# Kernel tuning notes

Measured on AMD Instinct MI355X. Metric: run time of the kernel, lower is better.

The kernel has to match this reference:

```python
import jax, jax.numpy as jnp
import numpy as np

N_NODES = 100000
N_GRAPHS = 256
EPS = 1e-5


def setup_inputs() -> dict:
    key = jax.random.key(0)
    ks = jax.random.split(key, 16)
    x = jax.random.normal(ks[0], (N_NODES, 7), dtype=jnp.float32)
    edge_index = jax.random.randint(ks[1], (2, 1600000), 0, N_NODES, dtype=jnp.int64)
    batch = jnp.sort(jax.random.randint(ks[2], (N_NODES,), 0, N_GRAPHS, dtype=jnp.int64))

    def lin(k, fi, fo):
        s = 1.0 / np.sqrt(fi)
        kw, kb = jax.random.split(k)
        W = jax.random.uniform(kw, (fi, fo), jnp.float32, -s, s)
        b = jax.random.uniform(kb, (fo,), jnp.float32, -s, s)
        return W, b

    W1, b1 = lin(ks[3], 7, 71)
    W2, b2 = lin(ks[4], 71, 135)
    W3, b3 = lin(ks[5], 135, 199)
    Wl1, bl1 = lin(ks[6], 199, 49)
    Wl2, bl2 = lin(ks[7], 49, 2)
    return {
        "x": x, "edge_index": edge_index, "batch": batch,
        "bn0_g": jnp.ones((7,)), "bn0_b": jnp.zeros((7,)),
        "bn1_g": jnp.ones((71,)), "bn1_b": jnp.zeros((71,)),
        "bn2_g": jnp.ones((135,)), "bn2_b": jnp.zeros((135,)),
        "W1": W1, "b1": b1, "W2": W2, "b2": b2, "W3": W3, "b3": b3,
        "Wl1": Wl1, "bl1": bl1, "Wl2": Wl2, "bl2": bl2,
    }


def _bn(x, g, b):
    # BatchNorm1d in training mode: batch stats over node dim
    m = jnp.mean(x, axis=0)
    v = jnp.mean(jnp.square(x - m), axis=0)
    return (x - m) * jax.lax.rsqrt(v + EPS) * g + b


def _gcn(x, src, dst, norm, W, b):
    # PyG GCNConv: x' = D^{-1/2} (A+I) D^{-1/2} (x W) + b
    h = x @ W
    out = jax.ops.segment_sum(norm[:, None] * h[src], dst, num_segments=N_NODES)
    return out + b


def reference(x, edge_index, batch, bn0_g, bn0_b, bn1_g, bn1_b, bn2_g, bn2_b,
              W1, b1, W2, b2, W3, b3, Wl1, bl1, Wl2, bl2):
    # add self loops
    loops = jnp.arange(N_NODES, dtype=edge_index.dtype)
    src = jnp.concatenate([edge_index[0], loops])
    dst = jnp.concatenate([edge_index[1], loops])
    deg = jax.ops.segment_sum(jnp.ones_like(dst, dtype=x.dtype), dst, num_segments=N_NODES)
    d_isqrt = jax.lax.rsqrt(jnp.maximum(deg, 1.0))
    norm = d_isqrt[src] * d_isqrt[dst]

    h = _bn(x, bn0_g, bn0_b)
    h = jax.nn.relu(_gcn(h, src, dst, norm, W1, b1))
    h = _bn(h, bn1_g, bn1_b)
    h = jax.nn.relu(_gcn(h, src, dst, norm, W2, b2))
    h = _bn(h, bn2_g, bn2_b)
    h = jax.nn.relu(_gcn(h, src, dst, norm, W3, b3))

    # global mean pool over graphs
    sums = jax.ops.segment_sum(h, batch, num_segments=N_GRAPHS)
    cnts = jax.ops.segment_sum(jnp.ones((h.shape[0],), h.dtype), batch, num_segments=N_GRAPHS)
    pooled = sums / jnp.maximum(cnts, 1.0)[:, None]

    out = pooled @ Wl1 + bl1
    out = out @ Wl2 + bl2
    return out
```

## Files before the change

### kernel.cpp

```cpp
#include <hip/hip_runtime.h>
#include <hip/hip_fp16.h>

#define EPSV 1e-5f
#define BIN_CH 4096
#define BCAP 8192

typedef _Float16 f16;
typedef f16 half8 __attribute__((ext_vector_type(8)));
typedef float f32x4 __attribute__((ext_vector_type(4)));


__global__ __launch_bounds__(256) void k_bin(const int* __restrict__ src,
                                             const int* __restrict__ dst, int E, int EN,
                                             int NBK, int* __restrict__ gcur,
                                             int* __restrict__ binned) {
    __shared__ int cnt[512];
    __shared__ int base[512];
    for (int b = threadIdx.x; b < 512; b += 256) cnt[b] = 0;
    __syncthreads();
    int i0 = blockIdx.x * BIN_CH;
    int i1 = i0 + BIN_CH; if (i1 > EN) i1 = EN;
    for (int i = i0 + threadIdx.x; i < i1; i += 256) {
        int d = (i < E) ? dst[i] : (i - E);
        atomicAdd(&cnt[d >> 8], 1);
    }
    __syncthreads();
    for (int b = threadIdx.x; b < NBK; b += 256)
        if (cnt[b]) base[b] = b * BCAP + atomicAdd(&gcur[b], cnt[b]);
    __syncthreads();
    for (int i = i0 + threadIdx.x; i < i1; i += 256) {
        int s, d;
        if (i < E) { s = src[i]; d = dst[i]; }
        else       { s = i - E; d = s; }
        int pos = atomicAdd(&base[d >> 8], 1);
        binned[pos] = s | ((d & 255) << 24);
    }
}

__global__ __launch_bounds__(256) void k_bucket(const int* __restrict__ binned,
                                                const int* __restrict__ gcur, int N,
                                                int* __restrict__ deg, int* __restrict__ rs,
                                                int* __restrict__ csr_s,
                                                float* __restrict__ disq) {
    __shared__ int deg_l[256];
    __shared__ int sc[256];
    __shared__ int cur_l[256];
    int b = blockIdx.x;
    int t = threadIdx.x;
    int start = b * BCAP, end = start + gcur[b];
    deg_l[t] = 0;
    __syncthreads();
    for (int i = start + t; i < end; i += 256)
        atomicAdd(&deg_l[((unsigned)binned[i]) >> 24], 1);
    __syncthreads();
    sc[t] = deg_l[t];
    __syncthreads();
    for (int off = 1; off < 256; off <<= 1) {
        int v = (t >= off) ? sc[t - off] : 0;
        __syncthreads();
        sc[t] += v;
        __syncthreads();
    }
    int rs_l = sc[t] - deg_l[t];
    int n = b * 256 + t;
    if (n < N) {
        deg[n] = deg_l[t];
        rs[n] = start + rs_l;
        disq[n] = rsqrtf((float)(deg_l[t] > 0 ? deg_l[t] : 1));
    }
    cur_l[t] = start + rs_l;
    __syncthreads();
    for (int i = start + t; i < end; i += 256) {
        int p = binned[i];
        int loc = ((unsigned)p) >> 24;
        int idx = atomicAdd(&cur_l[loc], 1);
        csr_s[idx] = p & 0xFFFFFF;
    }
}

__global__ __launch_bounds__(256) void k_wfill(const int* __restrict__ rs,
                                               const int* __restrict__ deg,
                                               const int* __restrict__ csr_s,
                                               const float* __restrict__ disq,
                                               int2* __restrict__ csr_sw, int N) {
    int wave = threadIdx.x >> 6, lane = threadIdx.x & 63;
    int n = blockIdx.x * 4 + wave;
    if (n >= N) return;
    int e0 = rs[n], dg = deg[n];
    float dn = disq[n];
    for (int j = lane; j < dg; j += 64) {
        int s = csr_s[e0 + j];
        int2 sw;
        sw.x = s;
        sw.y = __float_as_int(disq[s] * dn);
        csr_sw[e0 + j] = sw;
    }
}


__global__ __launch_bounds__(256) void k_prep(
    const float* __restrict__ colsum, const float* __restrict__ colsq,
    const float* __restrict__ g, const float* __restrict__ b, float invN,
    const float* __restrict__ W, int Cin, int Cout, int KP,
    f16* __restrict__ Wp, float* __restrict__ wrow) {
    __shared__ float lsc[192];
    __shared__ float lsh[192];
    __shared__ float red[4];
    int t = threadIdx.x;
    int c = blockIdx.x;
    if (t < KP) {
        float scv = 0.f, shv = 0.f;
        if (t < Cin) {
            float m = colsum[t] * invN;
            float v = colsq[t] * invN - m * m;
            float rstd = rsqrtf(fmaxf(v, 0.f) + EPSV);
            scv = rstd * g[t];
            shv = b[t] - m * scv;
        }
        lsc[t] = scv; lsh[t] = shv;
    }
    __syncthreads();
    float part = 0.f;
    if (t < KP) {
        float wv = (t < Cin && c < Cout) ? W[(size_t)t * Cout + c] : 0.f;
        Wp[(size_t)c * KP + t] = (f16)(lsc[t] * wv);
        part = lsh[t] * wv;
    }
    for (int off = 32; off > 0; off >>= 1) part += __shfl_down(part, off);
    int lane = t & 63, wid = t >> 6;
    if (lane == 0) red[wid] = part;
    __syncthreads();
    if (t == 0) wrow[c] = red[0] + red[1] + red[2] + red[3];
}


__global__ __launch_bounds__(256) void k_padx_stats(const float* __restrict__ x,
                                                    __half* __restrict__ xp, int N,
                                                    float* __restrict__ colsum,
                                                    float* __restrict__ colsq,
                                                    const int* __restrict__ batch,
                                                    int* __restrict__ gstart,
                                                    int* __restrict__ gend) {
    __shared__ float ls[16];
    int t = threadIdx.x;
    int n = blockIdx.x * 256 + t;
    int lane = t & 63;
    if (t < 16) ls[t] = 0.f;
    __syncthreads();
    float v[7] = {0.f, 0.f, 0.f, 0.f, 0.f, 0.f, 0.f};
    if (n < N) {
#pragma unroll
        for (int j = 0; j < 7; ++j) v[j] = x[(size_t)n * 7 + j];
        __half h[8];
#pragma unroll
        for (int j = 0; j < 7; ++j) h[j] = __float2half(v[j]);
        h[7] = __float2half(0.f);
        *(float4*)(xp + (size_t)n * 8) = *(float4*)h;
        int g = batch[n];
        int gp = (n == 0) ? -1 : batch[n - 1];
        if (gp != g) gstart[g] = n;
        int gn = (n == N - 1) ? -1 : batch[n + 1];
        if (gn != g) gend[g] = n + 1;
    }
#pragma unroll
    for (int j = 0; j < 7; ++j) {
        float s = v[j];
        float q = v[j] * v[j];
        for (int off = 32; off > 0; off >>= 1) {
            s += __shfl_down(s, off);
            q += __shfl_down(q, off);
        }
        if (lane == 0) {
            atomicAdd(&ls[j], s);
            atomicAdd(&ls[8 + j], q);
        }
    }
    __syncthreads();
    if (t < 8)               atomicAdd(&colsum[t], ls[t]);
    else if (t < 16)         atomicAdd(&colsq[t - 8], ls[t]);
}

__device__ __forceinline__ void fma8(float* acc, float w, float4 r) {
    float2 q0 = __half22float2(((const __half2*)&r)[0]);
    float2 q1 = __half22float2(((const __half2*)&r)[1]);
    float2 q2 = __half22float2(((const __half2*)&r)[2]);
    float2 q3 = __half22float2(((const __half2*)&r)[3]);
    acc[0] = fmaf(w, q0.x, acc[0]); acc[1] = fmaf(w, q0.y, acc[1]);
    acc[2] = fmaf(w, q1.x, acc[2]); acc[3] = fmaf(w, q1.y, acc[3]);
    acc[4] = fmaf(w, q2.x, acc[4]); acc[5] = fmaf(w, q2.y, acc[5]);
    acc[6] = fmaf(w, q3.x, acc[6]); acc[7] = fmaf(w, q3.y, acc[7]);
}

__device__ __forceinline__ void gather_walk(const __half* __restrict__ gb, int SPM,
                                            const int2* __restrict__ csr_sw,
                                            int e0, int eend, float* acc) {
    if (e0 >= eend) return;
    int2 cur[8];
#pragma unroll
    for (int i = 0; i < 8; ++i) cur[i] = csr_sw[e0 + i];
    for (int e = e0; e < eend; ) {
        int en = e + 8;
        int2 nxt[8];
#pragma unroll
        for (int i = 0; i < 8; ++i) nxt[i] = csr_sw[en + i];
        float4 r[8];
#pragma unroll
        for (int i = 0; i < 8; ++i) {
            int si = (e + i < eend) ? cur[i].x : 0;
            r[i] = *(const float4*)(gb + (size_t)si * SPM);
        }
#pragma unroll
        for (int i = 0; i < 8; ++i) {
            float w = (e + i < eend) ? __int_as_float(cur[i].y) : 0.f;
            fma8(acc, w, r[i]);
        }
#pragma unroll
        for (int i = 0; i < 8; ++i) cur[i] = nxt[i];
        e = en;
    }
}


__global__ __launch_bounds__(256) void k_fused1(
    const __half* __restrict__ xp, const f16* __restrict__ Bt,
    const int* __restrict__ rs, const int* __restrict__ deg,
    const int2* __restrict__ csr_sw,
    const float* __restrict__ wrow, const float* __restrict__ bias,
    f16* __restrict__ outM, f16* __restrict__ outT,
    float* __restrict__ colsum, float* __restrict__ colsq,
    float* __restrict__ rsum, int N) {
    const int COUT = 71;
    __shared__ f16 As[32][40];
    __shared__ float rsum_l[32];
    const int r0 = blockIdx.x * 32;
    const int t = threadIdx.x;
    const int wave = t >> 6, lane = t & 63;
    const int l15 = lane & 15, quad = lane >> 4;

    {
        float4 z = {0.f, 0.f, 0.f, 0.f};
        for (int i = t; i < 32 * 40 / 8; i += 256) ((float4*)As)[i] = z;
    }
    __syncthreads();

    {
        int lrow = wave * 8 + (lane >> 3);
        int sl = lane & 7;
        int n = r0 + lrow;
        float acc[8] = {};
        float ws = 0.f;
        if (n < N) {
            int eend = rs[n] + deg[n];
            for (int e = rs[n] + sl; e < eend; e += 8) {
                int2 sw = csr_sw[e];
                float w = __int_as_float(sw.y);
                ws += w;
                fma8(acc, w, *(const float4*)(xp + (size_t)sw.x * 8));
            }
        }
#pragma unroll
        for (int j = 0; j < 8; ++j) {
            acc[j] += __shfl_xor(acc[j], 1);
            acc[j] += __shfl_xor(acc[j], 2);
            acc[j] += __shfl_xor(acc[j], 4);
        }
        ws += __shfl_xor(ws, 1); ws += __shfl_xor(ws, 2); ws += __shfl_xor(ws, 4);
        if (sl == 0) {
            __half2 h[4];
            h[0] = __floats2half2_rn(acc[0], acc[1]);
            h[1] = __floats2half2_rn(acc[2], acc[3]);
            h[2] = __floats2half2_rn(acc[4], acc[5]);
            h[3] = __floats2half2_rn(acc[6], acc[7]);
            *(float4*)&As[lrow][0] = *(float4*)h;
            rsum_l[lrow] = ws;
            if (n < N) rsum[n] = ws;
        }
    }
    __syncthreads();

    for (int c16 = wave; c16 < 5; c16 += 4) {
        const int gc = c16 * 16 + l15;
        f32x4 zero4 = {0.f, 0.f, 0.f, 0.f};
        f32x4 acc2[2] = {zero4, zero4};
        half8 b = *(const half8*)(Bt + (size_t)gc * 32 + quad * 8);
#pragma unroll
        for (int mg = 0; mg < 2; ++mg) {
            half8 a = *(const half8*)&As[mg * 16 + l15][quad * 8];
            acc2[mg] = __builtin_amdgcn_mfma_f32_16x16x32_f16(a, b, acc2[mg], 0, 0, 0);
        }
        float wr1 = wrow[gc];
        float bi1 = (gc < COUT) ? bias[gc] : 0.f;
        float ps = 0.f, pq = 0.f;
#pragma unroll
        for (int mg = 0; mg < 2; ++mg) {
#pragma unroll
            for (int reg = 0; reg < 4; ++reg) {
                int lrow = mg * 16 + quad * 4 + reg;
                int gr = r0 + lrow;
                float o = acc2[mg][reg] + rsum_l[lrow] * wr1 + bi1;
                o = fmaxf(o, 0.f);
                if (gc >= COUT || gr >= N) o = 0.f;
                ps += o; pq += o * o;
                if (gr < N) {
                    if (gc < 64)      outM[(size_t)gr * 64 + gc] = (f16)o;
                    else if (gc < 72) outT[(size_t)gr * 8 + (gc - 64)] = (f16)o;
                }
            }
        }
        ps += __shfl_down(ps, 32); ps += __shfl_down(ps, 16);
        pq += __shfl_down(pq, 32); pq += __shfl_down(pq, 16);
        if (lane < 16 && gc < COUT) {
            atomicAdd(&colsum[gc], ps);
            atomicAdd(&colsq[gc], pq);
        }
    }
}


__global__ __launch_bounds__(256) void k_fused2(
    const __half* __restrict__ Am, const __half* __restrict__ At,
    const f16* __restrict__ Bt,
    const int* __restrict__ rs, const int* __restrict__ deg,
    const int2* __restrict__ csr_sw,
    const float* __restrict__ rsum, const float* __restrict__ wrow,
    const float* __restrict__ bias,
    f16* __restrict__ outM, f16* __restrict__ outT,
    float* __restrict__ colsum, float* __restrict__ colsq, int N) {
    const int KP = 96, SPM = 64, COUT = 135;
    __shared__ f16 As[32][104];
    __shared__ float rsum_l[32];
    const int r0 = blockIdx.x * 32;
    const int t = threadIdx.x;
    const int wave = t >> 6, lane = t & 63;
    const int l15 = lane & 15, quad = lane >> 4;

    if (t < 32) rsum_l[t] = (r0 + t < N) ? rsum[r0 + t] : 0.f;
    {
        float4 z = {0.f, 0.f, 0.f, 0.f};
        for (int i = t; i < 32 * 104 / 8; i += 256) ((float4*)As)[i] = z;
    }
    __syncthreads();

    {
        int lrow = wave * 8 + (lane >> 3);
        const __half* gb = Am + (lane & 7) * 8;
        int n = r0 + lrow;
        float acc[8] = {};
        if (n < N) gather_walk(gb, SPM, csr_sw, rs[n], rs[n] + deg[n], acc);
        __half2 h[4];
        h[0] = __floats2half2_rn(acc[0], acc[1]);
        h[1] = __floats2half2_rn(acc[2], acc[3]);
        h[2] = __floats2half2_rn(acc[4], acc[5]);
        h[3] = __floats2half2_rn(acc[6], acc[7]);
        *(float4*)&As[lrow][(lane & 7) * 8] = *(float4*)h;
    }
    {
        int lrow = wave * 8 + (lane >> 3);
        int sl = lane & 7;
        int n = r0 + lrow;
        float acc[8] = {};
        if (n < N) {
            int eend = rs[n] + deg[n];
            for (int e = rs[n] + sl; e < eend; e += 8) {
                int2 sw = csr_sw[e];
                fma8(acc, __int_as_float(sw.y), *(const float4*)(At + (size_t)sw.x * 8));
            }
        }
#pragma unroll
        for (int j = 0; j < 8; ++j) {
            acc[j] += __shfl_xor(acc[j], 1);
            acc[j] += __shfl_xor(acc[j], 2);
            acc[j] += __shfl_xor(acc[j], 4);
        }
        if (sl == 0) {
            __half2 h[4];
            h[0] = __floats2half2_rn(acc[0], acc[1]);
            h[1] = __floats2half2_rn(acc[2], acc[3]);
            h[2] = __floats2half2_rn(acc[4], acc[5]);
            h[3] = __floats2half2_rn(acc[6], acc[7]);
            *(float4*)&As[lrow][64] = *(float4*)h;
        }
    }
    __syncthreads();

    for (int c16 = wave; c16 < 9; c16 += 4) {
        const int gc = c16 * 16 + l15;
        f32x4 zero4 = {0.f, 0.f, 0.f, 0.f};
        f32x4 acc2[2] = {zero4, zero4};
#pragma unroll
        for (int kt = 0; kt < 3; ++kt) {
            int k0 = kt * 32;
            half8 b = *(const half8*)(Bt + (size_t)gc * KP + k0 + quad * 8);
#pragma unroll
            for (int mg = 0; mg < 2; ++mg) {
                half8 a = *(const half8*)&As[mg * 16 + l15][k0 + quad * 8];
                acc2[mg] = __builtin_amdgcn_mfma_f32_16x16x32_f16(a, b, acc2[mg], 0, 0, 0);
            }
        }
        float wr1 = wrow[gc];
        float bi1 = (gc < COUT) ? bias[gc] : 0.f;
        float ps = 0.f, pq = 0.f;
#pragma unroll
        for (int mg = 0; mg < 2; ++mg) {
#pragma unroll
            for (int reg = 0; reg < 4; ++reg) {
                int lrow = mg * 16 + quad * 4 + reg;
                int gr = r0 + lrow;
                float o = acc2[mg][reg] + rsum_l[lrow] * wr1 + bi1;
                o = fmaxf(o, 0.f);
                if (gc >= COUT || gr >= N) o = 0.f;
                ps += o; pq += o * o;
                if (gr < N) {
                    if (gc < 128)      outM[(size_t)gr * 128 + gc] = (f16)o;
                    else if (gc < 136) outT[(size_t)gr * 8 + (gc - 128)] = (f16)o;
                }
            }
        }
        ps += __shfl_down(ps, 32); ps += __shfl_down(ps, 16);
        pq += __shfl_down(pq, 32); pq += __shfl_down(pq, 16);
        if (lane < 16 && gc < COUT) {
            atomicAdd(&colsum[gc], ps);
            atomicAdd(&colsq[gc], pq);
        }
    }
}


__global__ __launch_bounds__(256) void k_fused3(
    const __half* __restrict__ Am, const __half* __restrict__ At,
    const f16* __restrict__ Bt,
    const int* __restrict__ rs, const int* __restrict__ deg,
    const int2* __restrict__ csr_sw,
    const float* __restrict__ rsum, const float* __restrict__ wrow,
    const float* __restrict__ bias, const int* __restrict__ batch,
    float* __restrict__ pooled, int N) {
    const int KP = 160, SPM = 128, COUT = 199;
    __shared__ f16 As[32][168];
    __shared__ int sbat[32];
    __shared__ float rsum_l[32];
    const int r0 = blockIdx.x * 32;
    const int t = threadIdx.x;
    const int wave = t >> 6, lane = t & 63;
    const int l15 = lane & 15, quad = lane >> 4;

    if (t < 32) {
        int gr = r0 + t;
        sbat[t] = batch[(gr < N) ? gr : (N - 1)];
        rsum_l[t] = (gr < N) ? rsum[gr] : 0.f;
    }
    {
        float4 z = {0.f, 0.f, 0.f, 0.f};
        for (int i = t; i < 32 * 168 / 8; i += 256) ((float4*)As)[i] = z;
    }
    __syncthreads();

    {
        const int sub = lane >> 4, lsub = lane & 15;
        const __half* gb = Am + lsub * 8;
        for (int pass = 0; pass < 2; ++pass) {
            int lrow = wave * 8 + pass * 4 + sub;
            int n = r0 + lrow;
            float acc[8] = {};
            if (n < N) gather_walk(gb, SPM, csr_sw, rs[n], rs[n] + deg[n], acc);
            __half2 h[4];
            h[0] = __floats2half2_rn(acc[0], acc[1]);
            h[1] = __floats2half2_rn(acc[2], acc[3]);
            h[2] = __floats2half2_rn(acc[4], acc[5]);
            h[3] = __floats2half2_rn(acc[6], acc[7]);
            *(float4*)&As[lrow][lsub * 8] = *(float4*)h;
        }
    }
    {
        int lrow = wave * 8 + (lane >> 3);
        int sl = lane & 7;
        int n = r0 + lrow;
        float acc[8] = {};
        if (n < N) {
            int eend = rs[n] + deg[n];
            for (int e = rs[n] + sl; e < eend; e += 8) {
                int2 sw = csr_sw[e];
                fma8(acc, __int_as_float(sw.y), *(const float4*)(At + (size_t)sw.x * 8));
            }
        }
#pragma unroll
        for (int j = 0; j < 8; ++j) {
            acc[j] += __shfl_xor(acc[j], 1);
            acc[j] += __shfl_xor(acc[j], 2);
            acc[j] += __shfl_xor(acc[j], 4);
        }
        if (sl == 0) {
            __half2 h[4];
            h[0] = __floats2half2_rn(acc[0], acc[1]);
            h[1] = __floats2half2_rn(acc[2], acc[3]);
            h[2] = __floats2half2_rn(acc[4], acc[5]);
            h[3] = __floats2half2_rn(acc[6], acc[7]);
            *(float4*)&As[lrow][128] = *(float4*)h;
        }
    }
    __syncthreads();

    const int g0 = sbat[0];
    const int ng = sbat[31] - g0;
    unsigned gpack = 0;
#pragma unroll
    for (int i = 0; i < 8; ++i) {
        int lrow = (i >> 2) * 16 + quad * 4 + (i & 3);
        gpack |= (unsigned)(sbat[lrow] - g0) << (2 * i);
    }

    for (int c16 = wave; c16 < 13; c16 += 4) {
        const int gc = c16 * 16 + l15;
        f32x4 zero4 = {0.f, 0.f, 0.f, 0.f};
        f32x4 acc2[2] = {zero4, zero4};
#pragma unroll
        for (int kt = 0; kt < 5; ++kt) {
            int k0 = kt * 32;
            half8 b = *(const half8*)(Bt + (size_t)gc * KP + k0 + quad * 8);
#pragma unroll
            for (int mg = 0; mg < 2; ++mg) {
                half8 a = *(const half8*)&As[mg * 16 + l15][k0 + quad * 8];
                acc2[mg] = __builtin_amdgcn_mfma_f32_16x16x32_f16(a, b, acc2[mg], 0, 0, 0);
            }
        }
        float wr1 = wrow[gc];
        float bi1 = (gc < COUT) ? bias[gc] : 0.f;
#pragma unroll
        for (int mg = 0; mg < 2; ++mg) {
#pragma unroll
            for (int reg = 0; reg < 4; ++reg) {
                int lrow = mg * 16 + quad * 4 + reg;
                bool rok = (r0 + lrow < N);
                float o = acc2[mg][reg] + rsum_l[lrow] * wr1 + bi1;
                o = fmaxf(o, 0.f);
                acc2[mg][reg] = (rok && gc < COUT) ? o : 0.f;
            }
        }
        for (int gg = 0; gg <= ng; ++gg) {
            float p = 0.f;
#pragma unroll
            for (int i = 0; i < 8; ++i) {
                bool m = (((gpack >> (2 * i)) & 3u) == (unsigned)gg);
                p += m ? acc2[i >> 2][i & 3] : 0.f;
            }
            p += __shfl_down(p, 32); p += __shfl_down(p, 16);
            if (lane < 16 && gc < COUT && p != 0.f)
                atomicAdd(&pooled[(size_t)(g0 + gg) * COUT + gc], p);
        }
    }
}


__global__ void k_mlp(const float* __restrict__ pooled, const int* __restrict__ gstart,
                      const int* __restrict__ gend,
                      const float* __restrict__ Wl1, const float* __restrict__ bl1,
                      const float* __restrict__ Wl2, const float* __restrict__ bl2,
                      float* __restrict__ out, int C) {
    __shared__ float p[199];
    __shared__ float t1[49];
    int g = blockIdx.x;
    int cnt = gend[g] - gstart[g];
    float inv = 1.f / (float)(cnt > 1 ? cnt : 1);
    for (int k = threadIdx.x; k < C; k += blockDim.x) p[k] = pooled[g * C + k] * inv;
    __syncthreads();
    if (threadIdx.x < 49) {
        float acc = bl1[threadIdx.x];
        for (int k = 0; k < C; ++k) acc += p[k] * Wl1[k * 49 + threadIdx.x];
        t1[threadIdx.x] = acc;
    }
    __syncthreads();
    if (threadIdx.x < 2) {
        float acc = bl2[threadIdx.x];
        for (int k = 0; k < 49; ++k) acc += t1[k] * Wl2[k * 2 + threadIdx.x];
        out[g * 2 + threadIdx.x] = acc;
    }
}


extern "C" void kernel_launch(void* const* d_in, const int* in_sizes, int n_in,
                              void* d_out, int out_size, void* d_ws, size_t ws_size,
                              hipStream_t stream) {
    const float* x     = (const float*)d_in[0];
    const int*   ei    = (const int*)d_in[1];
    const int*   batch = (const int*)d_in[2];
    const float* bn0g = (const float*)d_in[3];
    const float* bn0b = (const float*)d_in[4];
    const float* bn1g = (const float*)d_in[5];
    const float* bn1b = (const float*)d_in[6];
    const float* bn2g = (const float*)d_in[7];
    const float* bn2b = (const float*)d_in[8];
    const float* W1  = (const float*)d_in[9];
    const float* b1  = (const float*)d_in[10];
    const float* W2  = (const float*)d_in[11];
    const float* b2  = (const float*)d_in[12];
    const float* W3  = (const float*)d_in[13];
    const float* b3  = (const float*)d_in[14];
    const float* Wl1 = (const float*)d_in[15];
    const float* bl1 = (const float*)d_in[16];
    const float* Wl2 = (const float*)d_in[17];
    const float* bl2 = (const float*)d_in[18];

    const int N = in_sizes[0] / 7;
    const int E = in_sizes[1] / 2;
    const int EN = E + N;
    const int G = out_size / 2;
    const int NB = (N + 255) / 256;
    const int NBK = (N + 255) / 256;
    const int NBIN = (EN + BIN_CH - 1) / BIN_CH;

    const int* src = ei;
    const int* dst = ei + E;

    char* w = (char*)d_ws;
    auto alloc = [&](size_t bytes) -> void* {
        void* p = (void*)w;
        w += ((bytes + 255) / 256) * 256;
        return p;
    };
    size_t szH1m = (size_t)N * 64 * sizeof(__half);
    size_t szH1t = (size_t)N * 8 * sizeof(__half);
    size_t szH2m = (size_t)N * 128 * sizeof(__half);
    size_t szH2t = (size_t)N * 8 * sizeof(__half);
    char* regA = (char*)alloc(szH1m + szH1t + szH2m + szH2t);
    __half* H1m = (__half*)regA;
    __half* H1t = (__half*)(regA + szH1m);
    __half* H2m = (__half*)(regA + szH1m + szH1t);
    __half* H2t = (__half*)(regA + szH1m + szH1t + szH2m);

    f16*    wp   = (f16*)  alloc((size_t)256 * 160 * sizeof(f16));
    float*  wrow = (float*)alloc(256 * sizeof(float));
    __half* xp   = (__half*)alloc((size_t)N * 8 * sizeof(__half));
    float* disq  = (float*)alloc((size_t)N * sizeof(float));
    float* rsum  = (float*)alloc((size_t)N * sizeof(float));
    int*   deg   = (int*)  alloc((size_t)N * sizeof(int));
    int*   rs    = (int*)  alloc((size_t)N * sizeof(int));
    int*   binned= (int*)  alloc((size_t)NBK * BCAP * sizeof(int));
    int*   csr_s = (int*)  alloc((size_t)NBK * BCAP * sizeof(int));
    int2*  csr_sw= (int2*) alloc((size_t)NBK * BCAP * sizeof(int2) + 256);
    float* colsum0 = (float*)alloc(256 * sizeof(float));
    float* colsq0  = (float*)alloc(256 * sizeof(float));
    float* colsumA = (float*)alloc(256 * sizeof(float));
    float* colsqA  = (float*)alloc(256 * sizeof(float));
    float* colsumB = (float*)alloc(256 * sizeof(float));
    float* colsqB  = (float*)alloc(256 * sizeof(float));
    int*   gcur    = (int*)  alloc(512 * sizeof(int));
    float* pooled  = (float*)alloc((size_t)G * 199 * sizeof(float));
    int*   gstart  = (int*)  alloc((size_t)G * sizeof(int));
    int*   gend    = (int*)  alloc((size_t)G * sizeof(int));

    size_t zbytes = 6 * 1024 + 2048 + (((size_t)G * 199 * sizeof(float) + 255) / 256) * 256;
    hipMemsetAsync(colsum0, 0, zbytes, stream);

    k_bin<<<NBIN, 256, 0, stream>>>(src, dst, E, EN, NBK, gcur, binned);
    k_bucket<<<NBK, 256, 0, stream>>>(binned, gcur, N, deg, rs, csr_s, disq);
    k_wfill<<<(N + 3) / 4, 256, 0, stream>>>(rs, deg, csr_s, disq, csr_sw, N);

    const int GB32 = (N + 31) / 32;

    k_padx_stats<<<NB, 256, 0, stream>>>(x, xp, N, colsum0, colsq0, batch, gstart, gend);
    k_prep<<<128, 256, 0, stream>>>(colsum0, colsq0, bn0g, bn0b, 1.f / (float)N,
                                    W1, 7, 71, 32, wp, wrow);
    k_fused1<<<GB32, 256, 0, stream>>>(xp, wp, rs, deg, csr_sw, wrow, b1,
                                       (f16*)H1m, (f16*)H1t, colsumA, colsqA, rsum, N);
    k_prep<<<192, 256, 0, stream>>>(colsumA, colsqA, bn1g, bn1b, 1.f / (float)N,
                                    W2, 71, 135, 96, wp, wrow);
    k_fused2<<<GB32, 256, 0, stream>>>(H1m, H1t, wp, rs, deg, csr_sw,
                                       rsum, wrow, b2, (f16*)H2m, (f16*)H2t,
                                       colsumB, colsqB, N);
    k_prep<<<256, 256, 0, stream>>>(colsumB, colsqB, bn2g, bn2b, 1.f / (float)N,
                                    W3, 135, 199, 160, wp, wrow);
    k_fused3<<<GB32, 256, 0, stream>>>(H2m, H2t, wp, rs, deg, csr_sw,
                                       rsum, wrow, b3, batch, pooled, N);

    k_mlp<<<G, 64, 0, stream>>>(pooled, gstart, gend, Wl1, bl1, Wl2, bl2, (float*)d_out, 199);
}
```

Measured before the change: 502.8 us.

## Use 64-row tiles in fused layer-2/3 kernels with wave-owned column blocks

The fused gather+GEMM kernels for layers 2 and 3 now process 64 nodes per block instead of 32. Each wave owns a contiguous column block across all four 16-row MFMA groups, so every B fragment load is reused four times, and layer 3 issues two B tiles per k-step. The tail-column gather now uses 4 lanes per row instead of 8. The aim is to cut the block count and redundant weight loads. In exchange, each block needs twice the shared memory and more registers, and in layer 2 one wave computes columns that are all padding.

```diff
diff --git a/kernel.cpp b/kernel.cpp
--- a/kernel.cpp
+++ b/kernel.cpp
@@ -326,42 +326,45 @@
     const float* __restrict__ bias,
     f16* __restrict__ outM, f16* __restrict__ outT,
     float* __restrict__ colsum, float* __restrict__ colsq, int N) {
-    const int KP = 96, SPM = 64, COUT = 135;
-    __shared__ f16 As[32][104];
-    __shared__ float rsum_l[32];
-    const int r0 = blockIdx.x * 32;
+    const int KP = 96, ASW = 104, SPM = 64, COUT = 135;
+    __shared__ f16 As[64][104];
+    __shared__ float rsum_l[64];
+    const int r0 = blockIdx.x * 64;
     const int t = threadIdx.x;
     const int wave = t >> 6, lane = t & 63;
     const int l15 = lane & 15, quad = lane >> 4;
 
-    if (t < 32) rsum_l[t] = (r0 + t < N) ? rsum[r0 + t] : 0.f;
+    if (t < 64) rsum_l[t] = (r0 + t < N) ? rsum[r0 + t] : 0.f;
     {
         float4 z = {0.f, 0.f, 0.f, 0.f};
-        for (int i = t; i < 32 * 104 / 8; i += 256) ((float4*)As)[i] = z;
+        for (int i = t; i < 64 * ASW / 8; i += 256) ((float4*)As)[i] = z;
     }
     __syncthreads();
 
     {
-        int lrow = wave * 8 + (lane >> 3);
-        const __half* gb = Am + (lane & 7) * 8;
-        int n = r0 + lrow;
-        float acc[8] = {};
-        if (n < N) gather_walk(gb, SPM, csr_sw, rs[n], rs[n] + deg[n], acc);
-        __half2 h[4];
-        h[0] = __floats2half2_rn(acc[0], acc[1]);
-        h[1] = __floats2half2_rn(acc[2], acc[3]);
-        h[2] = __floats2half2_rn(acc[4], acc[5]);
-        h[3] = __floats2half2_rn(acc[6], acc[7]);
-        *(float4*)&As[lrow][(lane & 7) * 8] = *(float4*)h;
+        const int sub = lane >> 3, lsub = lane & 7;
+        const __half* gb = Am + lsub * 8;
+        for (int pass = 0; pass < 2; ++pass) {
+            int lrow = wave * 16 + pass * 8 + sub;
+            int n = r0 + lrow;
+            float acc[8] = {};
+            if (n < N) gather_walk(gb, SPM, csr_sw, rs[n], rs[n] + deg[n], acc);
+            __half2 h[4];
+            h[0] = __floats2half2_rn(acc[0], acc[1]);
+            h[1] = __floats2half2_rn(acc[2], acc[3]);
+            h[2] = __floats2half2_rn(acc[4], acc[5]);
+            h[3] = __floats2half2_rn(acc[6], acc[7]);
+            *(float4*)&As[lrow][lsub * 8] = *(float4*)h;
+        }
     }
     {
-        int lrow = wave * 8 + (lane >> 3);
-        int sl = lane & 7;
+        const int p = lane >> 2, sl = lane & 3;
+        int lrow = wave * 16 + p;
         int n = r0 + lrow;
         float acc[8] = {};
         if (n < N) {
             int eend = rs[n] + deg[n];
-            for (int e = rs[n] + sl; e < eend; e += 8) {
+            for (int e = rs[n] + sl; e < eend; e += 4) {
                 int2 sw = csr_sw[e];
                 fma8(acc, __int_as_float(sw.y), *(const float4*)(At + (size_t)sw.x * 8));
             }
@@ -370,7 +373,6 @@
         for (int j = 0; j < 8; ++j) {
             acc[j] += __shfl_xor(acc[j], 1);
             acc[j] += __shfl_xor(acc[j], 2);
-            acc[j] += __shfl_xor(acc[j], 4);
         }
         if (sl == 0) {
             __half2 h[4];
@@ -383,16 +385,18 @@
     }
     __syncthreads();
 
-    for (int c16 = wave; c16 < 9; c16 += 4) {
-        const int gc = c16 * 16 + l15;
+    for (int ch = 0; ch < 3; ++ch) {
+        const int gc = wave * 48 + ch * 16 + l15;
         f32x4 zero4 = {0.f, 0.f, 0.f, 0.f};
-        f32x4 acc2[2] = {zero4, zero4};
+        f32x4 acc2[4];
+#pragma unroll
+        for (int mg = 0; mg < 4; ++mg) acc2[mg] = zero4;
 #pragma unroll
         for (int kt = 0; kt < 3; ++kt) {
             int k0 = kt * 32;
             half8 b = *(const half8*)(Bt + (size_t)gc * KP + k0 + quad * 8);
 #pragma unroll
-            for (int mg = 0; mg < 2; ++mg) {
+            for (int mg = 0; mg < 4; ++mg) {
                 half8 a = *(const half8*)&As[mg * 16 + l15][k0 + quad * 8];
                 acc2[mg] = __builtin_amdgcn_mfma_f32_16x16x32_f16(a, b, acc2[mg], 0, 0, 0);
             }
@@ -401,7 +405,7 @@
         float bi1 = (gc < COUT) ? bias[gc] : 0.f;
         float ps = 0.f, pq = 0.f;
 #pragma unroll
-        for (int mg = 0; mg < 2; ++mg) {
+        for (int mg = 0; mg < 4; ++mg) {
 #pragma unroll
             for (int reg = 0; reg < 4; ++reg) {
                 int lrow = mg * 16 + quad * 4 + reg;
@@ -434,31 +438,31 @@
     const float* __restrict__ rsum, const float* __restrict__ wrow,
     const float* __restrict__ bias, const int* __restrict__ batch,
     float* __restrict__ pooled, int N) {
-    const int KP = 160, SPM = 128, COUT = 199;
-    __shared__ f16 As[32][168];
-    __shared__ int sbat[32];
-    __shared__ float rsum_l[32];
-    const int r0 = blockIdx.x * 32;
+    const int KP = 160, ASW = 168, SPM = 128, COUT = 199;
+    __shared__ f16 As[64][168];
+    __shared__ int sbat[64];
+    __shared__ float rsum_l[64];
+    const int r0 = blockIdx.x * 64;
     const int t = threadIdx.x;
     const int wave = t >> 6, lane = t & 63;
     const int l15 = lane & 15, quad = lane >> 4;
 
-    if (t < 32) {
+    if (t < 64) {
         int gr = r0 + t;
         sbat[t] = batch[(gr < N) ? gr : (N - 1)];
         rsum_l[t] = (gr < N) ? rsum[gr] : 0.f;
     }
     {
         float4 z = {0.f, 0.f, 0.f, 0.f};
-        for (int i = t; i < 32 * 168 / 8; i += 256) ((float4*)As)[i] = z;
+        for (int i = t; i < 64 * ASW / 8; i += 256) ((float4*)As)[i] = z;
     }
     __syncthreads();
 
     {
         const int sub = lane >> 4, lsub = lane & 15;
         const __half* gb = Am + lsub * 8;
-        for (int pass = 0; pass < 2; ++pass) {
-            int lrow = wave * 8 + pass * 4 + sub;
+        for (int pass = 0; pass < 4; ++pass) {
+            int lrow = wave * 16 + pass * 4 + sub;
             int n = r0 + lrow;
             float acc[8] = {};
             if (n < N) gather_walk(gb, SPM, csr_sw, rs[n], rs[n] + deg[n], acc);
@@ -471,13 +475,13 @@
         }
     }
     {
-        int lrow = wave * 8 + (lane >> 3);
-        int sl = lane & 7;
+        const int p = lane >> 2, sl = lane & 3;
+        int lrow = wave * 16 + p;
         int n = r0 + lrow;
         float acc[8] = {};
         if (n < N) {
             int eend = rs[n] + deg[n];
-            for (int e = rs[n] + sl; e < eend; e += 8) {
+            for (int e = rs[n] + sl; e < eend; e += 4) {
                 int2 sw = csr_sw[e];
                 fma8(acc, __int_as_float(sw.y), *(const float4*)(At + (size_t)sw.x * 8));
             }
@@ -486,7 +490,6 @@
         for (int j = 0; j < 8; ++j) {
             acc[j] += __shfl_xor(acc[j], 1);
             acc[j] += __shfl_xor(acc[j], 2);
-            acc[j] += __shfl_xor(acc[j], 4);
         }
         if (sl == 0) {
             __half2 h[4];
@@ -500,51 +503,75 @@
     __syncthreads();
 
     const int g0 = sbat[0];
-    const int ng = sbat[31] - g0;
+    const int ng = sbat[63] - g0;
     unsigned gpack = 0;
 #pragma unroll
-    for (int i = 0; i < 8; ++i) {
+    for (int i = 0; i < 16; ++i) {
         int lrow = (i >> 2) * 16 + quad * 4 + (i & 3);
         gpack |= (unsigned)(sbat[lrow] - g0) << (2 * i);
     }
 
-    for (int c16 = wave; c16 < 13; c16 += 4) {
-        const int gc = c16 * 16 + l15;
+    for (int ch = 0; ch < 2; ++ch) {
+        const int cb = wave * 64 + ch * 32;
         f32x4 zero4 = {0.f, 0.f, 0.f, 0.f};
-        f32x4 acc2[2] = {zero4, zero4};
+        f32x4 acc2[4][2];
+#pragma unroll
+        for (int mg = 0; mg < 4; ++mg) {
+            acc2[mg][0] = zero4; acc2[mg][1] = zero4;
+        }
 #pragma unroll
         for (int kt = 0; kt < 5; ++kt) {
             int k0 = kt * 32;
-            half8 b = *(const half8*)(Bt + (size_t)gc * KP + k0 + quad * 8);
-#pragma unroll
-            for (int mg = 0; mg < 2; ++mg) {
+            half8 b0 = *(const half8*)(Bt + (size_t)(cb + l15) * KP + k0 + quad * 8);
+            half8 b1 = *(const half8*)(Bt + (size_t)(cb + 16 + l15) * KP + k0 + quad * 8);
+#pragma unroll
+            for (int mg = 0; mg < 4; ++mg) {
                 half8 a = *(const half8*)&As[mg * 16 + l15][k0 + quad * 8];
-                acc2[mg] = __builtin_amdgcn_mfma_f32_16x16x32_f16(a, b, acc2[mg], 0, 0, 0);
-            }
-        }
-        float wr1 = wrow[gc];
-        float bi1 = (gc < COUT) ? bias[gc] : 0.f;
-#pragma unroll
-        for (int mg = 0; mg < 2; ++mg) {
+                acc2[mg][0] = __builtin_amdgcn_mfma_f32_16x16x32_f16(a, b0, acc2[mg][0], 0, 0, 0);
+                acc2[mg][1] = __builtin_amdgcn_mfma_f32_16x16x32_f16(a, b1, acc2[mg][1], 0, 0, 0);
+            }
+        }
+        float wr[2], bi[2];
+        int gcn[2];
+#pragma unroll
+        for (int ni = 0; ni < 2; ++ni) {
+            gcn[ni] = cb + ni * 16 + l15;
+            wr[ni] = wrow[gcn[ni]];
+            bi[ni] = (gcn[ni] < COUT) ? bias[gcn[ni]] : 0.f;
+        }
+#pragma unroll
+        for (int mg = 0; mg < 4; ++mg) {
 #pragma unroll
             for (int reg = 0; reg < 4; ++reg) {
                 int lrow = mg * 16 + quad * 4 + reg;
                 bool rok = (r0 + lrow < N);
-                float o = acc2[mg][reg] + rsum_l[lrow] * wr1 + bi1;
-                o = fmaxf(o, 0.f);
-                acc2[mg][reg] = (rok && gc < COUT) ? o : 0.f;
+                float rsv = rsum_l[lrow];
+#pragma unroll
+                for (int ni = 0; ni < 2; ++ni) {
+                    float o = acc2[mg][ni][reg] + rsv * wr[ni] + bi[ni];
+                    o = fmaxf(o, 0.f);
+                    acc2[mg][ni][reg] = (rok && gcn[ni] < COUT) ? o : 0.f;
+                }
             }
         }
         for (int gg = 0; gg <= ng; ++gg) {
-            float p = 0.f;
-#pragma unroll
-            for (int i = 0; i < 8; ++i) {
+            float p0 = 0.f, p1 = 0.f;
+#pragma unroll
+            for (int i = 0; i < 16; ++i) {
                 bool m = (((gpack >> (2 * i)) & 3u) == (unsigned)gg);
-                p += m ? acc2[i >> 2][i & 3] : 0.f;
-            }
-            p += __shfl_down(p, 32); p += __shfl_down(p, 16);
-            if (lane < 16 && gc < COUT && p != 0.f)
-                atomicAdd(&pooled[(size_t)(g0 + gg) * COUT + gc], p);
+                int mg = i >> 2, reg = i & 3;
+                p0 += m ? acc2[mg][0][reg] : 0.f;
+                p1 += m ? acc2[mg][1][reg] : 0.f;
+            }
+            p0 += __shfl_down(p0, 32); p0 += __shfl_down(p0, 16);
+            p1 += __shfl_down(p1, 32); p1 += __shfl_down(p1, 16);
+            if (lane < 16) {
+                int g = g0 + gg;
+                if (gcn[0] < COUT && p0 != 0.f)
+                    atomicAdd(&pooled[(size_t)g * COUT + gcn[0]], p0);
+                if (gcn[1] < COUT && p1 != 0.f)
+                    atomicAdd(&pooled[(size_t)g * COUT + gcn[1]], p1);
+            }
         }
     }
 }
@@ -655,6 +682,7 @@
     k_wfill<<<(N + 3) / 4, 256, 0, stream>>>(rs, deg, csr_s, disq, csr_sw, N);
 
     const int GB32 = (N + 31) / 32;
+    const int GB64 = (N + 63) / 64;
 
     k_padx_stats<<<NB, 256, 0, stream>>>(x, xp, N, colsum0, colsq0, batch, gstart, gend);
     k_prep<<<128, 256, 0, stream>>>(colsum0, colsq0, bn0g, bn0b, 1.f / (float)N,
@@ -663,12 +691,12 @@
                                        (f16*)H1m, (f16*)H1t, colsumA, colsqA, rsum, N);
     k_prep<<<192, 256, 0, stream>>>(colsumA, colsqA, bn1g, bn1b, 1.f / (float)N,
                                     W2, 71, 135, 96, wp, wrow);
-    k_fused2<<<GB32, 256, 0, stream>>>(H1m, H1t, wp, rs, deg, csr_sw,
+    k_fused2<<<GB64, 256, 0, stream>>>(H1m, H1t, wp, rs, deg, csr_sw,
                                        rsum, wrow, b2, (f16*)H2m, (f16*)H2t,
                                        colsumB, colsqB, N);
     k_prep<<<256, 256, 0, stream>>>(colsumB, colsqB, bn2g, bn2b, 1.f / (float)N,
                                     W3, 135, 199, 160, wp, wrow);
-    k_fused3<<<GB32, 256, 0, stream>>>(H2m, H2t, wp, rs, deg, csr_sw,
+    k_fused3<<<GB64, 256, 0, stream>>>(H2m, H2t, wp, rs, deg, csr_sw,
                                        rsum, wrow, b3, batch, pooled, N);
 
     k_mlp<<<G, 64, 0, stream>>>(pooled, gstart, gend, Wl1, bl1, Wl2, bl2, (float*)d_out, 199);
```

Result: faster. 475.7 us (-5.4%).
